# Kernel optimization log

Measured on AMD Instinct MI355X. Metric: run time of the kernel, lower is better.

## Reference

```python
import jax, jax.numpy as jnp
import numpy as np

N_ITERS = 10
ETA = 0.1


def setup_inputs() -> dict:
    key = jax.random.key(0)
    k1, k2, k3 = jax.random.split(key, 3)
    u = jax.random.normal(k1, (65536, 512), dtype=jnp.float32)
    G_raw = jax.random.normal(k2, (512, 512), dtype=jnp.float32) * 0.01
    # log_lam initialized as log(0.5), matching lam_init=0.5
    log_lam = jnp.asarray(np.log(0.5), dtype=jnp.float32)
    return {"u": u, "G_raw": G_raw, "log_lam": log_lam}


def reference(u, G_raw, log_lam):
    lam = jnp.exp(log_lam)
    # symmetrize and zero the diagonal
    G = 0.5 * (G_raw + G_raw.T)
    G = G - jnp.diag(jnp.diagonal(G))

    def step(carry, _):
        v, a = carry
        dv = u - v - a @ G          # [N, dim]
        v = v + ETA * dv
        a = jnp.sign(v) * jax.nn.relu(jnp.abs(v) - lam)  # soft threshold
        return (v, a), None

    init = (jnp.zeros_like(u), jnp.zeros_like(u))
    (v, a), _ = jax.lax.scan(step, init, None, length=N_ITERS)
    return a
```

## Files before the change

### kernel.cpp

```cpp
#include <hip/hip_runtime.h>
#include <hip/hip_bf16.h>


typedef __attribute__((ext_vector_type(8))) short bf16x8;
typedef __attribute__((ext_vector_type(16))) float f32x16;

#define ETA 0.1f

__device__ __forceinline__ unsigned short f2bf(float f) {
  union { float f; unsigned u; } x; x.f = f;
  unsigned r = x.u + 0x7fffu + ((x.u >> 16) & 1u);
  return (unsigned short)(r >> 16);
}

__global__ void prep_G(const float* __restrict__ Graw, unsigned short* __restrict__ Gb) {
  int idx = blockIdx.x * blockDim.x + threadIdx.x;
  int k = idx >> 9, n = idx & 511;
  float g = 0.5f * (Graw[k * 512 + n] + Graw[n * 512 + k]);
  if (k == n) g = 0.f;
  int kk = k >> 4, ct = n >> 5;
  int lane = (n & 31) + (((k >> 3) & 1) << 5);
  int j = k & 7;
  Gb[((((kk * 16 + ct) * 64) + lane) << 3) + j] = f2bf(g);
}

__global__ __launch_bounds__(512, 2) void lca_kernel(
    const float* __restrict__ u_g, const unsigned short* __restrict__ Gb,
    const float* __restrict__ log_lam, float* __restrict__ out) {
  __shared__ unsigned short sA[64 * 520];

  const int tid = threadIdx.x;
  const int lane = tid & 63;
  const int wave = tid >> 6;
  const int R0 = blockIdx.x * 64;
  const int cl = lane & 31;
  const int rquad = (lane >> 5) * 4;
  const int C0 = wave * 64;

  const float lam = expf(log_lam[0]);

  f32x16 acc[2][2];
  f32x16 uu[2][2];

  #pragma unroll
  for (int rt = 0; rt < 2; ++rt) {
    #pragma unroll
    for (int ctl = 0; ctl < 2; ++ctl) {
      const float* base = u_g + (R0 + rt * 32 + rquad) * 512 + C0 + ctl * 32 + cl;
      f32x16 t;
      #pragma unroll
      for (int reg = 0; reg < 16; ++reg) {
        const int rofs = (reg & 3) + 8 * (reg >> 2);
        t[reg] = base[rofs * 512];
      }
      uu[rt][ctl] = t;
      acc[rt][ctl] = -t;
    }
  }

  auto epilogue = [&]() {
    #pragma unroll
    for (int rt = 0; rt < 2; ++rt) {
      #pragma unroll
      for (int ctl = 0; ctl < 2; ++ctl) {
        unsigned short* sa = &sA[(rt * 32 + rquad) * 520 + C0 + ctl * 32 + cl];
        #pragma unroll
        for (int reg = 0; reg < 16; ++reg) {
          const int rofs = (reg & 3) + 8 * (reg >> 2);
          float v = -ETA * acc[rt][ctl][reg];
          float av = copysignf(fmaxf(fabsf(v) - lam, 0.f), v);
          sa[rofs * 520] = f2bf(av);
        }
        acc[rt][ctl] = 0.9f * acc[rt][ctl] - uu[rt][ctl];
      }
    }
  };

  epilogue();
  __syncthreads();

  const unsigned short* paRow = sA + cl * 520 + ((lane >> 5) << 3);
  const bf16x8* gb = (const bf16x8*)Gb;
  const int bbase = wave * 2 * 64 + lane;

  #pragma unroll 1
  for (int t = 1; t < 10; ++t) {
    #pragma unroll 4
    for (int kk = 0; kk < 32; ++kk) {
      bf16x8 a0 = *(const bf16x8*)(paRow + kk * 16);
      bf16x8 a1 = *(const bf16x8*)(paRow + 32 * 520 + kk * 16);
      bf16x8 b0 = gb[bbase + kk * 1024];
      bf16x8 b1 = gb[bbase + kk * 1024 + 64];
      acc[0][0] = __builtin_amdgcn_mfma_f32_32x32x16_bf16(a0, b0, acc[0][0], 0, 0, 0);
      acc[0][1] = __builtin_amdgcn_mfma_f32_32x32x16_bf16(a0, b1, acc[0][1], 0, 0, 0);
      acc[1][0] = __builtin_amdgcn_mfma_f32_32x32x16_bf16(a1, b0, acc[1][0], 0, 0, 0);
      acc[1][1] = __builtin_amdgcn_mfma_f32_32x32x16_bf16(a1, b1, acc[1][1], 0, 0, 0);
    }
    __syncthreads();
    if (t < 9) {
      epilogue();
      __syncthreads();
    }
  }

  #pragma unroll
  for (int rt = 0; rt < 2; ++rt) {
    #pragma unroll
    for (int ctl = 0; ctl < 2; ++ctl) {
      float* ob = out + (R0 + rt * 32 + rquad) * 512 + C0 + ctl * 32 + cl;
      #pragma unroll
      for (int reg = 0; reg < 16; ++reg) {
        const int rofs = (reg & 3) + 8 * (reg >> 2);
        float v = -ETA * acc[rt][ctl][reg];
        ob[rofs * 512] = copysignf(fmaxf(fabsf(v) - lam, 0.f), v);
      }
    }
  }
}

extern "C" void kernel_launch(void* const* d_in, const int* in_sizes, int n_in,
                              void* d_out, int out_size, void* d_ws, size_t ws_size,
                              hipStream_t stream) {
  const float* u = (const float*)d_in[0];
  const float* Graw = (const float*)d_in[1];
  const float* log_lam = (const float*)d_in[2];
  float* out = (float*)d_out;
  unsigned short* Gb = (unsigned short*)d_ws;

  prep_G<<<dim3(1024), dim3(256), 0, stream>>>(Graw, Gb);
  lca_kernel<<<dim3(1024), dim3(512), 0, stream>>>(u, Gb, log_lam, out);
}
```

Baseline: 538.6 us.

## Use 128-row blocks, drop register-held u, stagger K order, add setprio

Each block now covers 128 rows with 16 waves arranged 2x8, so every B fragment fetched from global is reused across twice as many rows. The per-thread register copy of u is removed and u is re-read from global memory in each epilogue with nontemporal loads, which frees registers. The first iteration is folded into the initial load. The K loop start is offset per block group to spread contention on G, and MFMAs are wrapped in s_setprio. Output stores become nontemporal. In exchange, u is re-read every iteration, and the larger 130 KB LDS buffer with 1024-thread blocks may limit residency to one block per CU.

```diff
diff --git a/kernel.cpp b/kernel.cpp
--- a/kernel.cpp
+++ b/kernel.cpp
@@ -24,81 +24,87 @@
   Gb[((((kk * 16 + ct) * 64) + lane) << 3) + j] = f2bf(g);
 }
 
-__global__ __launch_bounds__(512, 2) void lca_kernel(
+__global__ __launch_bounds__(1024, 4) void lca_kernel(
     const float* __restrict__ u_g, const unsigned short* __restrict__ Gb,
     const float* __restrict__ log_lam, float* __restrict__ out) {
-  __shared__ unsigned short sA[64 * 520];
+  __shared__ unsigned short sA[128 * 520];
 
   const int tid = threadIdx.x;
   const int lane = tid & 63;
   const int wave = tid >> 6;
-  const int R0 = blockIdx.x * 64;
+  const int wr = wave >> 3;
+  const int wc = wave & 7;
+  const int R0 = blockIdx.x * 128;
   const int cl = lane & 31;
   const int rquad = (lane >> 5) * 4;
-  const int C0 = wave * 64;
+  const int s = (blockIdx.x >> 3) & 31;
 
   const float lam = expf(log_lam[0]);
 
   f32x16 acc[2][2];
-  f32x16 uu[2][2];
 
   #pragma unroll
   for (int rt = 0; rt < 2; ++rt) {
     #pragma unroll
     for (int ctl = 0; ctl < 2; ++ctl) {
-      const float* base = u_g + (R0 + rt * 32 + rquad) * 512 + C0 + ctl * 32 + cl;
-      f32x16 t;
+      const int lrow = wr * 64 + rt * 32 + rquad;
+      const int gcol = wc * 64 + ctl * 32 + cl;
+      const float* ub = u_g + (R0 + lrow) * 512 + gcol;
+      unsigned short* sa = &sA[lrow * 520 + gcol];
       #pragma unroll
       for (int reg = 0; reg < 16; ++reg) {
         const int rofs = (reg & 3) + 8 * (reg >> 2);
-        t[reg] = base[rofs * 512];
+        float uv = ub[rofs * 512];
+        float v = ETA * uv;
+        float av = copysignf(fmaxf(fabsf(v) - lam, 0.f), v);
+        sa[rofs * 520] = f2bf(av);
+        acc[rt][ctl][reg] = -1.9f * uv;
       }
-      uu[rt][ctl] = t;
-      acc[rt][ctl] = -t;
     }
   }
-
-  auto epilogue = [&]() {
-    #pragma unroll
-    for (int rt = 0; rt < 2; ++rt) {
-      #pragma unroll
-      for (int ctl = 0; ctl < 2; ++ctl) {
-        unsigned short* sa = &sA[(rt * 32 + rquad) * 520 + C0 + ctl * 32 + cl];
-        #pragma unroll
-        for (int reg = 0; reg < 16; ++reg) {
-          const int rofs = (reg & 3) + 8 * (reg >> 2);
-          float v = -ETA * acc[rt][ctl][reg];
-          float av = copysignf(fmaxf(fabsf(v) - lam, 0.f), v);
-          sa[rofs * 520] = f2bf(av);
-        }
-        acc[rt][ctl] = 0.9f * acc[rt][ctl] - uu[rt][ctl];
-      }
-    }
-  };
-
-  epilogue();
   __syncthreads();
 
-  const unsigned short* paRow = sA + cl * 520 + ((lane >> 5) << 3);
   const bf16x8* gb = (const bf16x8*)Gb;
-  const int bbase = wave * 2 * 64 + lane;
+  const int bb = (wc * 2) * 64 + lane;
+  const unsigned short* paRow = sA + (wr * 64 + cl) * 520 + ((lane >> 5) << 3);
 
   #pragma unroll 1
   for (int t = 1; t < 10; ++t) {
-    #pragma unroll 4
+    #pragma unroll 2
     for (int kk = 0; kk < 32; ++kk) {
-      bf16x8 a0 = *(const bf16x8*)(paRow + kk * 16);
-      bf16x8 a1 = *(const bf16x8*)(paRow + 32 * 520 + kk * 16);
-      bf16x8 b0 = gb[bbase + kk * 1024];
-      bf16x8 b1 = gb[bbase + kk * 1024 + 64];
+      const int kko = (kk + s) & 31;
+      bf16x8 b0 = gb[bb + kko * 1024];
+      bf16x8 b1 = gb[bb + kko * 1024 + 64];
+      bf16x8 a0 = *(const bf16x8*)(paRow + kko * 16);
+      bf16x8 a1 = *(const bf16x8*)(paRow + 32 * 520 + kko * 16);
+      __builtin_amdgcn_s_setprio(1);
       acc[0][0] = __builtin_amdgcn_mfma_f32_32x32x16_bf16(a0, b0, acc[0][0], 0, 0, 0);
       acc[0][1] = __builtin_amdgcn_mfma_f32_32x32x16_bf16(a0, b1, acc[0][1], 0, 0, 0);
       acc[1][0] = __builtin_amdgcn_mfma_f32_32x32x16_bf16(a1, b0, acc[1][0], 0, 0, 0);
       acc[1][1] = __builtin_amdgcn_mfma_f32_32x32x16_bf16(a1, b1, acc[1][1], 0, 0, 0);
+      __builtin_amdgcn_s_setprio(0);
     }
-    __syncthreads();
     if (t < 9) {
-      epilogue();
+      __syncthreads();
+      #pragma unroll
+      for (int rt = 0; rt < 2; ++rt) {
+        #pragma unroll
+        for (int ctl = 0; ctl < 2; ++ctl) {
+          const int lrow = wr * 64 + rt * 32 + rquad;
+          const int gcol = wc * 64 + ctl * 32 + cl;
+          const float* ub = u_g + (R0 + lrow) * 512 + gcol;
+          unsigned short* sa = &sA[lrow * 520 + gcol];
+          #pragma unroll
+          for (int reg = 0; reg < 16; ++reg) {
+            const int rofs = (reg & 3) + 8 * (reg >> 2);
+            float uv = __builtin_nontemporal_load(ub + rofs * 512);
+            float v = -ETA * acc[rt][ctl][reg];
+            float av = copysignf(fmaxf(fabsf(v) - lam, 0.f), v);
+            sa[rofs * 520] = f2bf(av);
+            acc[rt][ctl][reg] = 0.9f * acc[rt][ctl][reg] - uv;
+          }
+        }
+      }
       __syncthreads();
     }
   }
@@ -107,12 +113,15 @@
   for (int rt = 0; rt < 2; ++rt) {
     #pragma unroll
     for (int ctl = 0; ctl < 2; ++ctl) {
-      float* ob = out + (R0 + rt * 32 + rquad) * 512 + C0 + ctl * 32 + cl;
+      const int lrow = wr * 64 + rt * 32 + rquad;
+      const int gcol = wc * 64 + ctl * 32 + cl;
+      float* ob = out + (R0 + lrow) * 512 + gcol;
       #pragma unroll
       for (int reg = 0; reg < 16; ++reg) {
         const int rofs = (reg & 3) + 8 * (reg >> 2);
         float v = -ETA * acc[rt][ctl][reg];
-        ob[rofs * 512] = copysignf(fmaxf(fabsf(v) - lam, 0.f), v);
+        float av = copysignf(fmaxf(fabsf(v) - lam, 0.f), v);
+        __builtin_nontemporal_store(av, ob + rofs * 512);
       }
     }
   }
@@ -128,5 +137,5 @@
   unsigned short* Gb = (unsigned short*)d_ws;
 
   prep_G<<<dim3(1024), dim3(256), 0, stream>>>(Graw, Gb);
-  lca_kernel<<<dim3(1024), dim3(512), 0, stream>>>(u, Gb, log_lam, out);
+  lca_kernel<<<dim3(512), dim3(1024), 0, stream>>>(u, Gb, log_lam, out);
 }
```

New measurement: 789.6 us. 46.6% more time.
